# Optimization experiments

Hardware: AMD Instinct MI355X
Metric: run time of the kernel (lower is better)

Reference implementation:

```python
import jax, jax.numpy as jnp
import numpy as np
from jax import lax

B, T, V, E, H, K = 64, 512, 50000, 128, 256, 9


def setup_inputs() -> dict:
    key = jax.random.key(0)
    ks = jax.random.split(key, 18)
    def n(k, shape, s=0.1):
        return jax.random.normal(k, shape, dtype=jnp.float32) * s
    emb = n(ks[0], (V, E), 1.0).at[0].set(0.0)  # padding_idx=0 row zeroed
    return {
        'sentence': jax.random.randint(ks[1], (B, T), 0, V),
        'mask': jnp.ones((B, T), dtype=bool),
        'emb': emb,
        'Wih_f': n(ks[2], (4 * H, E)), 'Whh_f': n(ks[3], (4 * H, H)),
        'bih_f': n(ks[4], (4 * H,)), 'bhh_f': n(ks[5], (4 * H,)),
        'Wih_b': n(ks[6], (4 * H, E)), 'Whh_b': n(ks[7], (4 * H, H)),
        'bih_b': n(ks[8], (4 * H,)), 'bhh_b': n(ks[9], (4 * H,)),
        'Wout': n(ks[10], (K, 2 * H)), 'bout': n(ks[11], (K,)),
        'start': n(ks[12], (K,)), 'end': n(ks[13], (K,)), 'trans': n(ks[14], (K, K)),
        'h0': n(ks[15], (2, B, H), 1.0),  # torch randn init hidden, [layers*dirs,B,H]
        'c0': n(ks[16], (2, B, H), 1.0),
    }


def lstm_dir(x, Wih, Whh, bih, bhh, h0, c0, reverse):
    # x: [B,T,E]; PyTorch LSTM cell, gate order i,f,g,o
    bias = bih + bhh
    def cell(carry, xt):
        h, c = carry
        gates = xt @ Wih.T + h @ Whh.T + bias
        i, f, g, o = jnp.split(gates, 4, axis=-1)
        c = jax.nn.sigmoid(f) * c + jax.nn.sigmoid(i) * jnp.tanh(g)
        h = jax.nn.sigmoid(o) * jnp.tanh(c)
        return (h, c), h
    _, hs = lax.scan(cell, (h0, c0), x.swapaxes(0, 1), reverse=reverse)
    return hs.swapaxes(0, 1)  # [B,T,H]


def viterbi(feats, mask, start, end, trans):
    # feats: [B,T,K]; torchcrf _viterbi_decode (batch_first)
    score0 = start[None] + feats[:, 0]  # [B,K]
    def step(score, inp):
        e_t, m_t = inp  # [B,K], [B]
        br = score[:, :, None] + trans[None]        # [B,K_prev,K_next]
        nxt = jnp.max(br, axis=1) + e_t
        idx = jnp.argmax(br, axis=1)                # [B,K]
        new = jnp.where(m_t[:, None], nxt, score)
        return new, idx
    final, hist = lax.scan(step, score0,
                           (feats[:, 1:].swapaxes(0, 1), mask[:, 1:].swapaxes(0, 1)))
    final = final + end[None]
    best = jnp.max(final, -1)
    last = jnp.argmax(final, -1)  # [B]
    def back(tag, idx_t):
        prev = jnp.take_along_axis(idx_t, tag[:, None], 1)[:, 0]
        return prev, tag
    first, rest = lax.scan(back, last, hist, reverse=True)
    tags = jnp.concatenate([first[None], rest], 0).swapaxes(0, 1)  # [B,T]
    return tags.astype(jnp.int32), best


def reference(sentence, mask, emb, Wih_f, Whh_f, bih_f, bhh_f,
              Wih_b, Whh_b, bih_b, bhh_b, Wout, bout,
              start, end, trans, h0, c0):
    x = emb[sentence]  # [B,T,E]
    hf = lstm_dir(x, Wih_f, Whh_f, bih_f, bhh_f, h0[0], c0[0], False)
    hb = lstm_dir(x, Wih_b, Whh_b, bih_b, bhh_b, h0[1], c0[1], True)
    feats = jnp.concatenate([hf, hb], -1) @ Wout.T + bout  # [B,T,K]
    tags, _ = viterbi(feats, mask, start, end, trans)
    return tags
```

## Files before the change

### kernel.cpp

```cpp
#include <hip/hip_runtime.h>
#include <math.h>

#define BB 64
#define TT 512
#define EE 128
#define HH 256
#define NK 9

#define XROW 416
#define RKS  578

#define OFF_TICK  524288ULL
#define OFF_HS    528384ULL
#define OFF_FEATS (528384ULL + 134217728ULL)

__global__ void init_kernel(double* __restrict__ hx, int* __restrict__ tick,
                            const float* __restrict__ h0) {
  int gid = blockIdx.x * 256 + threadIdx.x;
  if (gid < 2 * HH * BB) {
    int d  = gid >> 14;
    int r  = gid & 16383;
    int bs = r >> 12;
    int bb = (r >> 8) & 15;
    int u  = r & 255;
    hx[(size_t)(d * 4 + bs) * 4096 + bb * 256 + u] =
        (double)h0[d * 16384 + (bs * 16 + bb) * 256 + u];
  }
  if (gid < 256) tick[gid] = 0;
}

__launch_bounds__(256, 1)
__global__ void recur_kernel(const int* __restrict__ sent, const float* __restrict__ emb,
                             const float* __restrict__ WihF, const float* __restrict__ WhhF,
                             const float* __restrict__ bihF, const float* __restrict__ bhhF,
                             const float* __restrict__ WihB, const float* __restrict__ WhhB,
                             const float* __restrict__ bihB, const float* __restrict__ bhhB,
                             const float* __restrict__ c0,
                             double* __restrict__ hx, int* __restrict__ tick,
                             double* __restrict__ hsout) {
  extern __shared__ double sm[];
  double* xh     = sm;
  double* red    = sm + 16 * XROW;
  double* bias_l = red + 16 * RKS;

  const int tid = threadIdx.x;
  const int g   = blockIdx.x & 7;
  const int dir = g >> 2;
  const int bs  = g & 3;
  const int u0  = (blockIdx.x >> 3) * 8;
  const int rr  = tid & 15;
  const int q   = tid >> 4;

  const float* Wih = dir ? WihB : WihF;
  const float* Whh = dir ? WhhB : WhhF;
  const float* bih = dir ? bihB : bihF;
  const float* bhh = dir ? bhhB : bhhF;

  const size_t g0 = (size_t)((rr >> 3) * HH + u0 + (rr & 7));
  const size_t g1 = g0 + 2 * (size_t)HH;
  double2 wx0[4], wx1[4], wh0[8], wh1[8];
  #pragma unroll
  for (int j = 0; j < 4; ++j) {
    wx0[j] = double2{(double)Wih[g0 * EE + q * 8 + 2 * j], (double)Wih[g0 * EE + q * 8 + 2 * j + 1]};
    wx1[j] = double2{(double)Wih[g1 * EE + q * 8 + 2 * j], (double)Wih[g1 * EE + q * 8 + 2 * j + 1]};
  }
  #pragma unroll
  for (int j = 0; j < 8; ++j) {
    wh0[j] = double2{(double)Whh[g0 * HH + q * 16 + 2 * j], (double)Whh[g0 * HH + q * 16 + 2 * j + 1]};
    wh1[j] = double2{(double)Whh[g1 * HH + q * 16 + 2 * j], (double)Whh[g1 * HH + q * 16 + 2 * j + 1]};
  }
  if (tid < 32) {
    int gr = (tid >> 3) * HH + u0 + (tid & 7);
    bias_l[tid] = (double)bih[gr] + (double)bhh[gr];
  }
  double creg = 0.0;
  if (rr < 8)
    creg = (double)c0[dir * (BB * HH) + (bs * 16 + q) * HH + u0 + rr];

  auto x_stage = [&](int tq) {
    int rank = q * 8 + (rr - 8);
    int bb_s = rank >> 3, cp = rank & 7;
    int tok = sent[(bs * 16 + bb_s) * TT + tq];
    const float4* ep = (const float4*)(emb + (size_t)tok * EE + cp * 16);
    double* dst = xh + bb_s * XROW + cp * 16;
    #pragma unroll
    for (int m = 0; m < 4; ++m) {
      float4 v = ep[m];
      dst[m * 4 + 0] = (double)v.x; dst[m * 4 + 1] = (double)v.y;
      dst[m * 4 + 2] = (double)v.z; dst[m * 4 + 3] = (double)v.w;
    }
  };

  int* cnt = tick + g * 32;

  if (rr >= 8) x_stage(dir ? TT - 1 : 0);
  __syncthreads();

  for (int i = 0; i < TT; ++i) {
    const int tq = dir ? (TT - 1 - i) : i;

    if (tid == 0) {
      const int tgt = 32 * i;
      while (__hip_atomic_load(cnt, __ATOMIC_RELAXED, __HIP_MEMORY_SCOPE_AGENT) < tgt) {}
    }
    __syncthreads();

    const double* hsrc = hx + (size_t)(((i & 1) * 2 + dir) * 4 + bs) * 4096;
    double hr[16];
    #pragma unroll
    for (int c = 0; c < 16; ++c)
      hr[c] = __hip_atomic_load(hsrc + c * 256 + tid,
                                __ATOMIC_RELAXED, __HIP_MEMORY_SCOPE_AGENT);

    double hp0[16], hp1[16];
    #pragma unroll
    for (int bb = 0; bb < 16; ++bb) {
      const double2* xr = (const double2*)(xh + bb * XROW + q * 8);
      double s0 = 0.0, s1 = 0.0;
      #pragma unroll
      for (int j = 0; j < 4; ++j) {
        double2 v = xr[j];
        s0 += v.x * wx0[j].x; s0 += v.y * wx0[j].y;
        s1 += v.x * wx1[j].x; s1 += v.y * wx1[j].y;
      }
      hp0[bb] = s0; hp1[bb] = s1;
    }

    #pragma unroll
    for (int c = 0; c < 16; ++c)
      xh[c * XROW + 128 + tid + 2 * (tid >> 4)] = hr[c];
    __syncthreads();

    #pragma unroll
    for (int bb = 0; bb < 16; ++bb) {
      const double2* hv = (const double2*)(xh + bb * XROW + 128 + 18 * q);
      double s0 = hp0[bb], s1 = hp1[bb];
      #pragma unroll
      for (int j = 0; j < 8; ++j) {
        double2 v = hv[j];
        s0 += v.x * wh0[j].x; s0 += v.y * wh0[j].y;
        s1 += v.x * wh1[j].x; s1 += v.y * wh1[j].y;
      }
      hp0[bb] = s0; hp1[bb] = s1;
    }

    #pragma unroll
    for (int p = 0; p < 8; ++p) {
      *(double2*)(red + q * RKS + rr * 18 + 2 * p)        = double2{hp0[2 * p], hp0[2 * p + 1]};
      *(double2*)(red + q * RKS + (rr + 16) * 18 + 2 * p) = double2{hp1[2 * p], hp1[2 * p + 1]};
    }
    __syncthreads();

    double su0 = bias_l[rr], su1 = bias_l[rr + 16];
    #pragma unroll
    for (int kk = 0; kk < 16; ++kk) {
      su0 += red[kk * RKS + rr * 18 + q];
      su1 += red[kk * RKS + (rr + 16) * 18 + q];
    }
    double p0 = __shfl_xor(su0, 8, 64);
    double p1 = __shfl_xor(su1, 8, 64);

    double hval = 0.0;
    if (rr < 8) {
      double iv = su0, gv = su1, fv = p0, ov = p1;
      double is = 1.0 / (1.0 + exp(-iv));
      double fs = 1.0 / (1.0 + exp(-fv));
      double gs = tanh(gv);
      double os = 1.0 / (1.0 + exp(-ov));
      creg = fs * creg + is * gs;
      hval = os * tanh(creg);
      __hip_atomic_store(hx + (size_t)((((i + 1) & 1) * 2 + dir) * 4 + bs) * 4096
                            + q * 256 + u0 + rr,
                         hval, __ATOMIC_RELAXED, __HIP_MEMORY_SCOPE_AGENT);
    } else if (i + 1 < TT) {
      x_stage(dir ? (TT - 2 - i) : (i + 1));
    }
    __syncthreads();

    if (tid == 0)
      __hip_atomic_fetch_add(cnt, 1, __ATOMIC_RELAXED, __HIP_MEMORY_SCOPE_AGENT);

    if (rr < 8)
      hsout[((size_t)(dir * TT + tq) * HH + u0 + rr) * 64 + bs * 16 + q] = hval;
  }
}

__global__ void feats_kernel(const double* __restrict__ hs, const float* __restrict__ Wout,
                             const float* __restrict__ bout, double* __restrict__ feats) {
  __shared__ double wl[NK * 2 * HH];
  __shared__ double bl[NK];
  int tid = threadIdx.x, t = blockIdx.x;
  for (int idx = tid; idx < NK * 2 * HH; idx += 256) wl[idx] = (double)Wout[idx];
  if (tid < NK) bl[tid] = (double)bout[tid];
  __syncthreads();
  if (tid < 192) {
    int bb = tid & 63, kg = tid >> 6;
    double acc0 = bl[kg * 3 + 0], acc1 = bl[kg * 3 + 1], acc2 = bl[kg * 3 + 2];
    for (int d = 0; d < 2; ++d) {
      const double* hp = hs + ((size_t)(d * TT + t) * HH) * 64 + bb;
      const double* w0 = wl + (kg * 3 + 0) * 2 * HH + d * HH;
      const double* w1 = wl + (kg * 3 + 1) * 2 * HH + d * HH;
      const double* w2 = wl + (kg * 3 + 2) * 2 * HH + d * HH;
      for (int u = 0; u < HH; ++u) {
        double hv = hp[(size_t)u * 64];
        acc0 += hv * w0[u];
        acc1 += hv * w1[u];
        acc2 += hv * w2[u];
      }
    }
    double* fp = feats + ((size_t)bb * TT + t) * NK + kg * 3;
    fp[0] = acc0; fp[1] = acc1; fp[2] = acc2;
  }
}

__global__ void viterbi_kernel(const double* __restrict__ feats, const float* __restrict__ start,
                               const float* __restrict__ endv, const float* __restrict__ trans,
                               int* __restrict__ out) {
  __shared__ double sc[NK];
  __shared__ double tr[NK * NK];
  __shared__ unsigned char hist[TT - 1][16];
  __shared__ unsigned char tags[TT];
  int lane = threadIdx.x, b = blockIdx.x;
  for (int idx = lane; idx < NK * NK; idx += 64) tr[idx] = (double)trans[idx];
  const double* fb = feats + (size_t)b * TT * NK;
  if (lane < NK) sc[lane] = (double)start[lane] + fb[lane];
  __syncthreads();
  double ftn = (lane < NK) ? fb[NK + lane] : 0.0;
  for (int t = 1; t < TT; ++t) {
    double ft = ftn;
    if (t + 1 < TT && lane < NK) ftn = fb[(size_t)(t + 1) * NK + lane];
    double best = -1e300; int arg = 0;
    if (lane < NK) {
      #pragma unroll
      for (int p = 0; p < NK; ++p) {
        double v = sc[p] + tr[p * NK + lane];
        if (v > best) { best = v; arg = p; }
      }
      hist[t - 1][lane] = (unsigned char)arg;
    }
    __syncthreads();
    if (lane < NK) sc[lane] = best + ft;
    __syncthreads();
  }
  if (lane < NK) sc[lane] += (double)endv[lane];
  __syncthreads();
  if (lane == 0) {
    double best = -1e300; int tag = 0;
    for (int n = 0; n < NK; ++n) if (sc[n] > best) { best = sc[n]; tag = n; }
    tags[TT - 1] = (unsigned char)tag;
    for (int t = TT - 2; t >= 0; --t) { tag = hist[t][tag]; tags[t] = (unsigned char)tag; }
  }
  __syncthreads();
  for (int j = lane; j < TT; j += 64) out[b * TT + j] = (int)tags[j];
}

extern "C" void kernel_launch(void* const* d_in, const int* in_sizes, int n_in,
                              void* d_out, int out_size, void* d_ws, size_t ws_size,
                              hipStream_t stream) {
  const int*   sent = (const int*)  d_in[0];
  const float* emb  = (const float*)d_in[2];
  const float* WihF = (const float*)d_in[3];
  const float* WhhF = (const float*)d_in[4];
  const float* bihF = (const float*)d_in[5];
  const float* bhhF = (const float*)d_in[6];
  const float* WihB = (const float*)d_in[7];
  const float* WhhB = (const float*)d_in[8];
  const float* bihB = (const float*)d_in[9];
  const float* bhhB = (const float*)d_in[10];
  const float* Wout = (const float*)d_in[11];
  const float* bout = (const float*)d_in[12];
  const float* stv  = (const float*)d_in[13];
  const float* env  = (const float*)d_in[14];
  const float* trv  = (const float*)d_in[15];
  const float* h0   = (const float*)d_in[16];
  const float* c0   = (const float*)d_in[17];

  char* ws = (char*)d_ws;
  double* hx    = (double*)ws;
  int*    tick  = (int*)(ws + OFF_TICK);
  double* hs    = (double*)(ws + OFF_HS);
  double* feats = (double*)(ws + OFF_FEATS);
  int* out = (int*)d_out;

  hipFuncSetAttribute((const void*)recur_kernel,
                      hipFuncAttributeMaxDynamicSharedMemorySize, 131072);

  init_kernel<<<128, 256, 0, stream>>>(hx, tick, h0);
  recur_kernel<<<256, 256, 127488, stream>>>(sent, emb, WihF, WhhF, bihF, bhhF,
                                             WihB, WhhB, bihB, bhhB, c0, hx, tick, hs);
  feats_kernel<<<TT, 256, 0, stream>>>(hs, Wout, bout, feats);
  viterbi_kernel<<<BB, 64, 0, stream>>>(feats, stv, env, trv, out);
}
```

Before: 4.029 ms.

## Replace LDS gate reduction with wave shuffle butterfly and hoist x-projection before barrier

Reworks the thread-to-gate mapping so each wave's 16 q-lanes hold partial sums for one gate row. The partials are then reduced with a transpose-style xor-shuffle butterfly instead of an LDS scratch buffer and an extra __syncthreads. The input-projection dot products now run before the cross-block spin-wait, so they overlap with waiting for the previous timestep's hidden state. LDS use shrinks considerably, at the cost of more shuffle and select instructions per step.

```diff
diff --git a/kernel.cpp b/kernel.cpp
--- a/kernel.cpp
+++ b/kernel.cpp
@@ -7,8 +7,10 @@
 #define HH 256
 #define NK 9
 
-#define XROW 416
-#define RKS  578
+#define XS_BB 162
+#define HS_BB 290
+#define HST_OFF (16 * XS_BB)
+#define LDS_DBL (HST_OFF + 16 * HS_BB)
 
 #define OFF_TICK  524288ULL
 #define OFF_HS    528384ULL
@@ -35,69 +37,85 @@
                              const float* __restrict__ bihF, const float* __restrict__ bhhF,
                              const float* __restrict__ WihB, const float* __restrict__ WhhB,
                              const float* __restrict__ bihB, const float* __restrict__ bhhB,
-                             const float* __restrict__ c0,
+                             const float* __restrict__ c0v,
                              double* __restrict__ hx, int* __restrict__ tick,
                              double* __restrict__ hsout) {
   extern __shared__ double sm[];
-  double* xh     = sm;
-  double* red    = sm + 16 * XROW;
-  double* bias_l = red + 16 * RKS;
-
-  const int tid = threadIdx.x;
-  const int g   = blockIdx.x & 7;
-  const int dir = g >> 2;
-  const int bs  = g & 3;
-  const int u0  = (blockIdx.x >> 3) * 8;
-  const int rr  = tid & 15;
-  const int q   = tid >> 4;
+  double* xs  = sm;
+  double* hst = sm + HST_OFF;
+
+  const int tid  = threadIdx.x;
+  const int g    = blockIdx.x & 7;
+  const int dir  = g >> 2;
+  const int bs   = g & 3;
+  const int u0   = (blockIdx.x >> 3) * 8;
+  const int w    = tid >> 6;
+  const int lane = tid & 63;
+  const int q    = lane & 15;
+  const int p    = lane >> 4;
+  const int rs   = w + 4 * p;
 
   const float* Wih = dir ? WihB : WihF;
   const float* Whh = dir ? WhhB : WhhF;
   const float* bih = dir ? bihB : bihF;
   const float* bhh = dir ? bhhB : bhhF;
 
-  const size_t g0 = (size_t)((rr >> 3) * HH + u0 + (rr & 7));
-  const size_t g1 = g0 + 2 * (size_t)HH;
+  const size_t r0 = (size_t)((rs >> 3) * HH + u0 + (rs & 7));
+  const size_t r1 = r0 + 2 * (size_t)HH;
   double2 wx0[4], wx1[4], wh0[8], wh1[8];
   #pragma unroll
   for (int j = 0; j < 4; ++j) {
-    wx0[j] = double2{(double)Wih[g0 * EE + q * 8 + 2 * j], (double)Wih[g0 * EE + q * 8 + 2 * j + 1]};
-    wx1[j] = double2{(double)Wih[g1 * EE + q * 8 + 2 * j], (double)Wih[g1 * EE + q * 8 + 2 * j + 1]};
+    wx0[j] = double2{(double)Wih[r0 * EE + q * 8 + 2 * j], (double)Wih[r0 * EE + q * 8 + 2 * j + 1]};
+    wx1[j] = double2{(double)Wih[r1 * EE + q * 8 + 2 * j], (double)Wih[r1 * EE + q * 8 + 2 * j + 1]};
   }
   #pragma unroll
   for (int j = 0; j < 8; ++j) {
-    wh0[j] = double2{(double)Whh[g0 * HH + q * 16 + 2 * j], (double)Whh[g0 * HH + q * 16 + 2 * j + 1]};
-    wh1[j] = double2{(double)Whh[g1 * HH + q * 16 + 2 * j], (double)Whh[g1 * HH + q * 16 + 2 * j + 1]};
-  }
-  if (tid < 32) {
-    int gr = (tid >> 3) * HH + u0 + (tid & 7);
-    bias_l[tid] = (double)bih[gr] + (double)bhh[gr];
-  }
+    wh0[j] = double2{(double)Whh[r0 * HH + q * 16 + 2 * j], (double)Whh[r0 * HH + q * 16 + 2 * j + 1]};
+    wh1[j] = double2{(double)Whh[r1 * HH + q * 16 + 2 * j], (double)Whh[r1 * HH + q * 16 + 2 * j + 1]};
+  }
+  const double bias0 = (double)bih[r0] + (double)bhh[r0];
+  const double bias1 = (double)bih[r1] + (double)bhh[r1];
+
   double creg = 0.0;
-  if (rr < 8)
-    creg = (double)c0[dir * (BB * HH) + (bs * 16 + q) * HH + u0 + rr];
+  if (p < 2)
+    creg = (double)c0v[dir * (BB * HH) + (bs * 16 + q) * HH + u0 + rs];
 
   auto x_stage = [&](int tq) {
-    int rank = q * 8 + (rr - 8);
-    int bb_s = rank >> 3, cp = rank & 7;
+    int rank = w * 32 + (p - 2) * 16 + q;
+    int bb_s = rank >> 3, qq = rank & 7;
     int tok = sent[(bs * 16 + bb_s) * TT + tq];
-    const float4* ep = (const float4*)(emb + (size_t)tok * EE + cp * 16);
-    double* dst = xh + bb_s * XROW + cp * 16;
-    #pragma unroll
-    for (int m = 0; m < 4; ++m) {
-      float4 v = ep[m];
-      dst[m * 4 + 0] = (double)v.x; dst[m * 4 + 1] = (double)v.y;
-      dst[m * 4 + 2] = (double)v.z; dst[m * 4 + 3] = (double)v.w;
-    }
+    const float4* ep = (const float4*)(emb + (size_t)tok * EE);
+    float4 v0 = ep[qq * 2], v1 = ep[qq * 2 + 1];
+    float4 v2 = ep[(qq + 8) * 2], v3 = ep[(qq + 8) * 2 + 1];
+    double* d0 = xs + bb_s * XS_BB + qq * 10;
+    double* d1 = xs + bb_s * XS_BB + (qq + 8) * 10;
+    d0[0] = (double)v0.x; d0[1] = (double)v0.y; d0[2] = (double)v0.z; d0[3] = (double)v0.w;
+    d0[4] = (double)v1.x; d0[5] = (double)v1.y; d0[6] = (double)v1.z; d0[7] = (double)v1.w;
+    d1[0] = (double)v2.x; d1[1] = (double)v2.y; d1[2] = (double)v2.z; d1[3] = (double)v2.w;
+    d1[4] = (double)v3.x; d1[5] = (double)v3.y; d1[6] = (double)v3.z; d1[7] = (double)v3.w;
   };
 
   int* cnt = tick + g * 32;
 
-  if (rr >= 8) x_stage(dir ? TT - 1 : 0);
+  if (p >= 2) x_stage(dir ? TT - 1 : 0);
   __syncthreads();
 
   for (int i = 0; i < TT; ++i) {
     const int tq = dir ? (TT - 1 - i) : i;
+
+    double hp0[16], hp1[16];
+    #pragma unroll
+    for (int bb = 0; bb < 16; ++bb) {
+      const double2* xr = (const double2*)(xs + bb * XS_BB + q * 10);
+      double s0 = 0.0, s1 = 0.0;
+      #pragma unroll
+      for (int j = 0; j < 4; ++j) {
+        double2 v = xr[j];
+        s0 += v.x * wx0[j].x; s0 += v.y * wx0[j].y;
+        s1 += v.x * wx1[j].x; s1 += v.y * wx1[j].y;
+      }
+      hp0[bb] = s0; hp1[bb] = s1;
+    }
 
     if (tid == 0) {
       const int tgt = 32 * i;
@@ -111,29 +129,14 @@
     for (int c = 0; c < 16; ++c)
       hr[c] = __hip_atomic_load(hsrc + c * 256 + tid,
                                 __ATOMIC_RELAXED, __HIP_MEMORY_SCOPE_AGENT);
-
-    double hp0[16], hp1[16];
+    #pragma unroll
+    for (int c = 0; c < 16; ++c)
+      hst[c * HS_BB + (tid >> 4) * 18 + (tid & 15)] = hr[c];
+    __syncthreads();
+
     #pragma unroll
     for (int bb = 0; bb < 16; ++bb) {
-      const double2* xr = (const double2*)(xh + bb * XROW + q * 8);
-      double s0 = 0.0, s1 = 0.0;
-      #pragma unroll
-      for (int j = 0; j < 4; ++j) {
-        double2 v = xr[j];
-        s0 += v.x * wx0[j].x; s0 += v.y * wx0[j].y;
-        s1 += v.x * wx1[j].x; s1 += v.y * wx1[j].y;
-      }
-      hp0[bb] = s0; hp1[bb] = s1;
-    }
-
-    #pragma unroll
-    for (int c = 0; c < 16; ++c)
-      xh[c * XROW + 128 + tid + 2 * (tid >> 4)] = hr[c];
-    __syncthreads();
-
-    #pragma unroll
-    for (int bb = 0; bb < 16; ++bb) {
-      const double2* hv = (const double2*)(xh + bb * XROW + 128 + 18 * q);
+      const double2* hv = (const double2*)(hst + bb * HS_BB + q * 18);
       double s0 = hp0[bb], s1 = hp1[bb];
       #pragma unroll
       for (int j = 0; j < 8; ++j) {
@@ -144,25 +147,61 @@
       hp0[bb] = s0; hp1[bb] = s1;
     }
 
-    #pragma unroll
-    for (int p = 0; p < 8; ++p) {
-      *(double2*)(red + q * RKS + rr * 18 + 2 * p)        = double2{hp0[2 * p], hp0[2 * p + 1]};
-      *(double2*)(red + q * RKS + (rr + 16) * 18 + 2 * p) = double2{hp1[2 * p], hp1[2 * p + 1]};
-    }
-    __syncthreads();
-
-    double su0 = bias_l[rr], su1 = bias_l[rr + 16];
-    #pragma unroll
-    for (int kk = 0; kk < 16; ++kk) {
-      su0 += red[kk * RKS + rr * 18 + q];
-      su1 += red[kk * RKS + (rr + 16) * 18 + q];
-    }
-    double p0 = __shfl_xor(su0, 8, 64);
-    double p1 = __shfl_xor(su1, 8, 64);
+    double sA[8], sB[8];
+    {
+      const int b = lane & 1;
+      #pragma unroll
+      for (int m = 0; m < 8; ++m) {
+        double k0 = b ? hp0[2 * m + 1] : hp0[2 * m];
+        double d0 = b ? hp0[2 * m]     : hp0[2 * m + 1];
+        sA[m] = k0 + __shfl_xor(d0, 1, 64);
+        double k1 = b ? hp1[2 * m + 1] : hp1[2 * m];
+        double d1 = b ? hp1[2 * m]     : hp1[2 * m + 1];
+        sB[m] = k1 + __shfl_xor(d1, 1, 64);
+      }
+    }
+    double tA[4], tB[4];
+    {
+      const int b = (lane >> 1) & 1;
+      #pragma unroll
+      for (int m = 0; m < 4; ++m) {
+        double k0 = b ? sA[2 * m + 1] : sA[2 * m];
+        double d0 = b ? sA[2 * m]     : sA[2 * m + 1];
+        tA[m] = k0 + __shfl_xor(d0, 2, 64);
+        double k1 = b ? sB[2 * m + 1] : sB[2 * m];
+        double d1 = b ? sB[2 * m]     : sB[2 * m + 1];
+        tB[m] = k1 + __shfl_xor(d1, 2, 64);
+      }
+    }
+    double uA[2], uB[2];
+    {
+      const int b = (lane >> 2) & 1;
+      #pragma unroll
+      for (int m = 0; m < 2; ++m) {
+        double k0 = b ? tA[2 * m + 1] : tA[2 * m];
+        double d0 = b ? tA[2 * m]     : tA[2 * m + 1];
+        uA[m] = k0 + __shfl_xor(d0, 4, 64);
+        double k1 = b ? tB[2 * m + 1] : tB[2 * m];
+        double d1 = b ? tB[2 * m]     : tB[2 * m + 1];
+        uB[m] = k1 + __shfl_xor(d1, 4, 64);
+      }
+    }
+    double su0, su1;
+    {
+      const int b = (lane >> 3) & 1;
+      double k0 = b ? uA[1] : uA[0];
+      double d0 = b ? uA[0] : uA[1];
+      su0 = k0 + __shfl_xor(d0, 8, 64) + bias0;
+      double k1 = b ? uB[1] : uB[0];
+      double d1 = b ? uB[0] : uB[1];
+      su1 = k1 + __shfl_xor(d1, 8, 64) + bias1;
+    }
+    double po0 = __shfl_xor(su0, 32, 64);
+    double po1 = __shfl_xor(su1, 32, 64);
 
     double hval = 0.0;
-    if (rr < 8) {
-      double iv = su0, gv = su1, fv = p0, ov = p1;
+    if (p < 2) {
+      double iv = su0, gv = su1, fv = po0, ov = po1;
       double is = 1.0 / (1.0 + exp(-iv));
       double fs = 1.0 / (1.0 + exp(-fv));
       double gs = tanh(gv);
@@ -170,7 +209,7 @@
       creg = fs * creg + is * gs;
       hval = os * tanh(creg);
       __hip_atomic_store(hx + (size_t)((((i + 1) & 1) * 2 + dir) * 4 + bs) * 4096
-                            + q * 256 + u0 + rr,
+                            + q * 256 + u0 + rs,
                          hval, __ATOMIC_RELAXED, __HIP_MEMORY_SCOPE_AGENT);
     } else if (i + 1 < TT) {
       x_stage(dir ? (TT - 2 - i) : (i + 1));
@@ -180,8 +219,8 @@
     if (tid == 0)
       __hip_atomic_fetch_add(cnt, 1, __ATOMIC_RELAXED, __HIP_MEMORY_SCOPE_AGENT);
 
-    if (rr < 8)
-      hsout[((size_t)(dir * TT + tq) * HH + u0 + rr) * 64 + bs * 16 + q] = hval;
+    if (p < 2)
+      hsout[((size_t)(dir * TT + tq) * HH + u0 + rs) * 64 + bs * 16 + q] = hval;
   }
 }
 
@@ -283,11 +322,11 @@
   int* out = (int*)d_out;
 
   hipFuncSetAttribute((const void*)recur_kernel,
-                      hipFuncAttributeMaxDynamicSharedMemorySize, 131072);
+                      hipFuncAttributeMaxDynamicSharedMemorySize, 65536);
 
   init_kernel<<<128, 256, 0, stream>>>(hx, tick, h0);
-  recur_kernel<<<256, 256, 127488, stream>>>(sent, emb, WihF, WhhF, bihF, bhhF,
-                                             WihB, WhhB, bihB, bhhB, c0, hx, tick, hs);
+  recur_kernel<<<256, 256, LDS_DBL * 8, stream>>>(sent, emb, WihF, WhhF, bihF, bhhF,
+                                                  WihB, WhhB, bihB, bhhB, c0, hx, tick, hs);
   feats_kernel<<<TT, 256, 0, stream>>>(hs, Wout, bout, feats);
   viterbi_kernel<<<BB, 64, 0, stream>>>(feats, stv, env, trv, out);
 }
```

After: 3.645 ms. -9.5%, faster.
